# Performance work log

Hardware: AMD Instinct MI355X
Metric: run time of the kernel (lower is better)

The kernel has to match this reference:

```python
import jax, jax.numpy as jnp
import numpy as np

N, DIM, H, E = 50000, 64, 8, 800000
NEG_SLOPE = 0.2


def setup_inputs() -> dict:
    key = jax.random.key(0)
    ks = jax.random.split(key, 6)
    x = jax.random.normal(ks[0], (N, DIM), dtype=jnp.float32)
    edge_index = jax.random.randint(ks[1], (2, E), 0, N, dtype=jnp.int32)
    # glorot-ish scaled params
    W = jax.random.normal(ks[2], (DIM, H * DIM), dtype=jnp.float32) * (1.0 / np.sqrt(DIM))
    att_src = jax.random.normal(ks[3], (H, DIM), dtype=jnp.float32) * (1.0 / np.sqrt(DIM))
    att_dst = jax.random.normal(ks[4], (H, DIM), dtype=jnp.float32) * (1.0 / np.sqrt(DIM))
    bias = jnp.zeros((DIM,), dtype=jnp.float32)
    return {"x": x, "edge_index": edge_index, "W": W, "att_src": att_src, "att_dst": att_dst, "bias": bias}


def reference(x, edge_index, W, att_src, att_dst, bias):
    n = x.shape[0]
    # PyG GATConv default: add self-loops
    loops = jnp.arange(n, dtype=edge_index.dtype)
    src = jnp.concatenate([edge_index[0], loops])  # [E+N]
    dst = jnp.concatenate([edge_index[1], loops])  # [E+N]
    # project: [N, H, C]
    h = (x @ W).reshape(n, H, DIM)
    # per-node attention contributions: [N, H]
    a_src = jnp.einsum("nhc,hc->nh", h, att_src)
    a_dst = jnp.einsum("nhc,hc->nh", h, att_dst)
    # per-edge logits with LeakyReLU: [E+N, H]
    logits = jax.nn.leaky_relu(a_src[src] + a_dst[dst], negative_slope=NEG_SLOPE)
    # segment softmax over incoming edges of each destination node
    seg_max = jax.ops.segment_max(logits, dst, num_segments=n)  # [N, H]
    seg_max = jnp.where(jnp.isfinite(seg_max), seg_max, 0.0)
    e = jnp.exp(logits - seg_max[dst])
    denom = jax.ops.segment_sum(e, dst, num_segments=n)  # [N, H]
    alpha = e / denom[dst]  # every node has a self-loop -> denom > 0
    # weighted messages and scatter-add: [E+N, H, C] -> [N, H, C]
    msg = h[src] * alpha[:, :, None]
    out = jax.ops.segment_sum(msg, dst, num_segments=n)
    # concat=False -> mean over heads, then bias
    return out.mean(axis=1) + bias
```

## Files before the change

### kernel.cpp

```cpp
#include <hip/hip_runtime.h>
#include <hip/hip_bf16.h>

#define NHEAD 8
#define KDIM 64
#define NCOL 512
#define NEG_SLOPE 0.2f
#define BUCKET 64
#define EPT 8

typedef short bf16x8 __attribute__((ext_vector_type(8)));
typedef float f32x4 __attribute__((ext_vector_type(4)));

__device__ inline float leaky(float x) { return fmaxf(x, NEG_SLOPE * x); }
__device__ inline float bf2f(unsigned short u) { return __uint_as_float(((unsigned)u) << 16); }
__device__ inline unsigned short f2bf(float f) {
    unsigned b = __float_as_uint(f);
    b += 0x7FFFu + ((b >> 16) & 1u);
    return (unsigned short)(b >> 16);
}

__global__ void k_wprep(const float* __restrict__ W, const float* __restrict__ att_src,
                        const float* __restrict__ att_dst,
                        float* __restrict__ WsT, float* __restrict__ WdT,
                        unsigned short* __restrict__ Bhi, unsigned short* __restrict__ Blo,
                        int* __restrict__ cur, int n) {
    int tid = blockIdx.x * 256 + threadIdx.x;
    for (int i = tid; i < n; i += 32768) cur[i] = 0;
    if (tid < NHEAD * KDIM) {
        int h = tid >> 6, k = tid & 63;
        float ps = 0.f, pd = 0.f;
        const float4* wp = (const float4*)(W + (size_t)k * NCOL + h * KDIM);
        const float4* sp = (const float4*)(att_src + h * KDIM);
        const float4* dp = (const float4*)(att_dst + h * KDIM);
        #pragma unroll
        for (int q = 0; q < KDIM / 4; ++q) {
            float4 wv = wp[q], sv = sp[q], dv = dp[q];
            ps += wv.x * sv.x + wv.y * sv.y + wv.z * sv.z + wv.w * sv.w;
            pd += wv.x * dv.x + wv.y * dv.y + wv.z * dv.z + wv.w * dv.w;
        }
        WsT[h * KDIM + k] = ps;
        WdT[h * KDIM + k] = pd;
    }
    if (tid < 4 * 16 * 64 * 8) {
        int j  = tid & 7;
        int l  = (tid >> 3) & 63;
        int kk = (tid >> 9) & 15;
        int ct = tid >> 13;
        int c  = ct * 16 + (l & 15);
        int hk = kk * 32 + ((l >> 4) << 3) + j;
        int h = hk >> 6, kx = hk & 63;
        float w = W[(size_t)kx * NCOL + h * KDIM + c];
        unsigned short hi = f2bf(w);
        Bhi[tid] = hi;
        Blo[tid] = f2bf(w - bf2f(hi));
    }
}

__global__ void k_xafill(const float* __restrict__ x,
                         const int* __restrict__ src, const int* __restrict__ dst,
                         const float* __restrict__ WsT, const float* __restrict__ WdT,
                         float* __restrict__ asrc, float* __restrict__ adst,
                         unsigned short* __restrict__ xb,
                         int* __restrict__ cur, unsigned short* __restrict__ bucket,
                         int n, int E, int nbx) {
    const int b = blockIdx.x;
    const int t = threadIdx.x;
    if (b < nbx) {
        int i = b * 256 + t;
        if (i >= n * NHEAD) return;
        int node = i >> 3, h = i & 7;
        const float4* xp = (const float4*)(x + (size_t)node * KDIM);
        const float4* sp = (const float4*)(WsT + h * KDIM);
        const float4* dp = (const float4*)(WdT + h * KDIM);
        float ps = 0.f, pd = 0.f;
        float4 kept0 = {0, 0, 0, 0}, kept1 = {0, 0, 0, 0};
        #pragma unroll
        for (int q = 0; q < KDIM / 4; ++q) {
            float4 xv = xp[q], sv = sp[q], dv = dp[q];
            if (q == 2 * h)     kept0 = xv;
            if (q == 2 * h + 1) kept1 = xv;
            ps += xv.x * sv.x + xv.y * sv.y + xv.z * sv.z + xv.w * sv.w;
            pd += xv.x * dv.x + xv.y * dv.y + xv.z * dv.z + xv.w * dv.w;
        }
        asrc[i] = ps;
        adst[i] = pd;
        ushort4 o0, o1;
        o0.x = f2bf(kept0.x); o0.y = f2bf(kept0.y); o0.z = f2bf(kept0.z); o0.w = f2bf(kept0.w);
        o1.x = f2bf(kept1.x); o1.y = f2bf(kept1.y); o1.z = f2bf(kept1.z); o1.w = f2bf(kept1.w);
        ushort4* op = (ushort4*)(xb + (size_t)node * KDIM + h * 8);
        op[0] = o0; op[1] = o1;
    } else {
        long long base = ((long long)(b - nbx) * 256 + t) * EPT;
        if (base + EPT <= E) {
            int4 d0 = *(const int4*)(dst + base);
            int4 d1 = *(const int4*)(dst + base + 4);
            int4 s0 = *(const int4*)(src + base);
            int4 s1 = *(const int4*)(src + base + 4);
            int dd[EPT] = {d0.x, d0.y, d0.z, d0.w, d1.x, d1.y, d1.z, d1.w};
            int ss[EPT] = {s0.x, s0.y, s0.z, s0.w, s1.x, s1.y, s1.z, s1.w};
            int pp[EPT];
            #pragma unroll
            for (int q = 0; q < EPT; ++q) pp[q] = atomicAdd(cur + dd[q], 1);
            #pragma unroll
            for (int q = 0; q < EPT; ++q)
                if (pp[q] < BUCKET)
                    bucket[(size_t)dd[q] * BUCKET + pp[q]] = (unsigned short)ss[q];
        } else {
            for (long long i = base; i < E; ++i) {
                int d = dst[i];
                int p = atomicAdd(cur + d, 1);
                if (p < BUCKET) bucket[(size_t)d * BUCKET + p] = (unsigned short)src[i];
            }
        }
    }
}

__global__ __launch_bounds__(256, 8) void k_aggproj(const unsigned short* __restrict__ bucket,
                                                    const int* __restrict__ cur,
                                                    const float* __restrict__ asrc,
                                                    const float* __restrict__ adst,
                                                    const unsigned short* __restrict__ xb,
                                                    const unsigned short* __restrict__ Bhi,
                                                    const unsigned short* __restrict__ Blo,
                                                    const float* __restrict__ bias,
                                                    float* __restrict__ out, int n) {
    __shared__ __align__(16) unsigned short Yh_l[16][520];

    const int t = threadIdx.x;
    const int w = t >> 6;
    const int lane = t & 63;
    const int base = blockIdx.x * 16;
    const int hg = lane >> 3;
    const int hLo = lane & 7;
    const int dly = (lane & 7) << 3;

#define PROCU(EV, RW)                                                          \
    {                                                                          \
        den += (EV);                                                           \
        uint4 u_ = (RW);                                                       \
        y[0] += (EV) * __uint_as_float(u_.x << 16);                            \
        y[1] += (EV) * __uint_as_float(u_.x & 0xFFFF0000u);                    \
        y[2] += (EV) * __uint_as_float(u_.y << 16);                            \
        y[3] += (EV) * __uint_as_float(u_.y & 0xFFFF0000u);                    \
        y[4] += (EV) * __uint_as_float(u_.z << 16);                            \
        y[5] += (EV) * __uint_as_float(u_.z & 0xFFFF0000u);                    \
        y[6] += (EV) * __uint_as_float(u_.w << 16);                            \
        y[7] += (EV) * __uint_as_float(u_.w & 0xFFFF0000u);                    \
    }

    for (int q = 0; q < 4; ++q) {
        const int row = w * 4 + q;
        int d = base + row;
        if (d >= n) d = n - 1;

        const float adLo = adst[(size_t)d * NHEAD + hLo];
        float den = 0.f;
        float y[8];
        #pragma unroll
        for (int i = 0; i < 8; ++i) y[i] = 0.f;

        int cnt = cur[d];
        cnt = cnt < BUCKET ? cnt : BUCKET;
        int sv = (lane < cnt) ? (int)bucket[(size_t)d * BUCKET + lane] : 0;

        {
            float asLo = asrc[(size_t)d * NHEAD + hLo];
            float evs = __expf(leaky(asLo + adLo));
            float e = __shfl(evs, hg);
            uint4 r = *(const uint4*)(xb + ((size_t)d << 6) + dly);
            PROCU(e, r)
        }

        int j = 0;
        for (; j + 4 <= cnt; j += 4) {
            int sb = __shfl(sv, j + ((lane >> 3) & 3));
            float ab = asrc[(size_t)sb * NHEAD + hLo];
            float ev = __expf(leaky(ab + adLo));
            int s0 = __shfl(sv, j);
            int s1 = __shfl(sv, j + 1);
            int s2 = __shfl(sv, j + 2);
            int s3 = __shfl(sv, j + 3);
            uint4 r0 = *(const uint4*)(xb + ((size_t)s0 << 6) + dly);
            uint4 r1 = *(const uint4*)(xb + ((size_t)s1 << 6) + dly);
            uint4 r2 = *(const uint4*)(xb + ((size_t)s2 << 6) + dly);
            uint4 r3 = *(const uint4*)(xb + ((size_t)s3 << 6) + dly);
            float e0 = __shfl(ev, 0 * 8 + hg);
            PROCU(e0, r0)
            float e1 = __shfl(ev, 1 * 8 + hg);
            PROCU(e1, r1)
            float e2 = __shfl(ev, 2 * 8 + hg);
            PROCU(e2, r2)
            float e3 = __shfl(ev, 3 * 8 + hg);
            PROCU(e3, r3)
        }
        for (; j < cnt; ++j) {
            int s = __shfl(sv, j);
            float a = asrc[(size_t)s * NHEAD + hLo];
            float evt = __expf(leaky(a + adLo));
            float e = __shfl(evt, hg);
            uint4 r = *(const uint4*)(xb + ((size_t)s << 6) + dly);
            PROCU(e, r)
        }

        float inv = 1.0f / den;
        ushort4 h0, h1;
        h0.x = f2bf(y[0] * inv); h0.y = f2bf(y[1] * inv);
        h0.z = f2bf(y[2] * inv); h0.w = f2bf(y[3] * inv);
        h1.x = f2bf(y[4] * inv); h1.y = f2bf(y[5] * inv);
        h1.z = f2bf(y[6] * inv); h1.w = f2bf(y[7] * inv);
        unsigned short* yh = &Yh_l[row][hg * KDIM + dly];
        ((ushort4*)yh)[0] = h0; ((ushort4*)yh)[1] = h1;
    }
#undef PROCU

    __syncthreads();

    const bf16x8* BH = (const bf16x8*)Bhi;
    const bf16x8* BL = (const bf16x8*)Blo;
    const int ar = lane & 15;
    const int ak = (lane >> 4) << 3;

    f32x4 acc = {0.f, 0.f, 0.f, 0.f};
    #pragma unroll
    for (int kk = 0; kk < 16; ++kk) {
        bf16x8 ah = *(const bf16x8*)&Yh_l[ar][kk * 32 + ak];
        bf16x8 bh = BH[(w * 16 + kk) * 64 + lane];
        bf16x8 bl = BL[(w * 16 + kk) * 64 + lane];
        acc = __builtin_amdgcn_mfma_f32_16x16x32_bf16(ah, bh, acc, 0, 0, 0);
        acc = __builtin_amdgcn_mfma_f32_16x16x32_bf16(ah, bl, acc, 0, 0, 0);
    }

    int col = w * 16 + (lane & 15);
    float b = bias[col];
    int rbase = base + ((lane >> 4) << 2);
    #pragma unroll
    for (int r = 0; r < 4; ++r) {
        int rowg = rbase + r;
        if (rowg < n) out[(size_t)rowg * KDIM + col] = acc[r] * 0.125f + b;
    }
}

extern "C" void kernel_launch(void* const* d_in, const int* in_sizes, int n_in,
                              void* d_out, int out_size, void* d_ws, size_t ws_size,
                              hipStream_t stream) {
    const float* x       = (const float*)d_in[0];
    const int*   ei      = (const int*)d_in[1];
    const float* W       = (const float*)d_in[2];
    const float* att_src = (const float*)d_in[3];
    const float* att_dst = (const float*)d_in[4];
    const float* bias    = (const float*)d_in[5];

    const int n = in_sizes[0] / KDIM;
    const int E = in_sizes[1] / 2;
    const int* src = ei;
    const int* dst = ei + E;

    char* w = (char*)d_ws;
    unsigned short* xb  = (unsigned short*)w;  w += (size_t)n * KDIM * 2;
    unsigned short* Bhi = (unsigned short*)w;  w += (size_t)32768 * 2;
    unsigned short* Blo = (unsigned short*)w;  w += (size_t)32768 * 2;
    float* WsT  = (float*)w;                   w += (size_t)NHEAD * KDIM * 4;
    float* WdT  = (float*)w;                   w += (size_t)NHEAD * KDIM * 4;
    float* asrc = (float*)w;                   w += (size_t)n * NHEAD * 4;
    float* adst = (float*)w;                   w += (size_t)n * NHEAD * 4;
    int*   cur  = (int*)w;                     w += (size_t)n * 4;
    unsigned short* bucket = (unsigned short*)w; w += (size_t)n * BUCKET * 2;

    k_wprep<<<128, 256, 0, stream>>>(W, att_src, att_dst, WsT, WdT, Bhi, Blo, cur, n);

    const int nbx = (n * NHEAD + 255) / 256;
    const int ethreads = (E + EPT - 1) / EPT;
    const int nbe = (ethreads + 255) / 256;
    k_xafill<<<nbx + nbe, 256, 0, stream>>>(x, src, dst, WsT, WdT, asrc, adst, xb,
                                            cur, bucket, n, E, nbx);

    k_aggproj<<<(n + 15) / 16, 256, 0, stream>>>(bucket, cur, asrc, adst, xb, Bhi, Blo,
                                                 bias, (float*)d_out, n);
}
```

Baseline: 146.0 us.

## Replace fixed-size per-node edge buckets with atomicExch linked lists

```diff
diff --git a/kernel.cpp b/kernel.cpp
--- a/kernel.cpp
+++ b/kernel.cpp
@@ -23,9 +23,9 @@
                         const float* __restrict__ att_dst,
                         float* __restrict__ WsT, float* __restrict__ WdT,
                         unsigned short* __restrict__ Bhi, unsigned short* __restrict__ Blo,
-                        int* __restrict__ cur, int n) {
+                        int* __restrict__ head, int n) {
     int tid = blockIdx.x * 256 + threadIdx.x;
-    for (int i = tid; i < n; i += 32768) cur[i] = 0;
+    for (int i = tid; i < n; i += 32768) head[i] = -1;
     if (tid < NHEAD * KDIM) {
         int h = tid >> 6, k = tid & 63;
         float ps = 0.f, pd = 0.f;
@@ -61,7 +61,7 @@
                          const float* __restrict__ WsT, const float* __restrict__ WdT,
                          float* __restrict__ asrc, float* __restrict__ adst,
                          unsigned short* __restrict__ xb,
-                         int* __restrict__ cur, unsigned short* __restrict__ bucket,
+                         int* __restrict__ head, int2* __restrict__ pairs,
                          int n, int E, int nbx) {
     const int b = blockIdx.x;
     const int t = threadIdx.x;
@@ -98,25 +98,27 @@
             int4 s1 = *(const int4*)(src + base + 4);
             int dd[EPT] = {d0.x, d0.y, d0.z, d0.w, d1.x, d1.y, d1.z, d1.w};
             int ss[EPT] = {s0.x, s0.y, s0.z, s0.w, s1.x, s1.y, s1.z, s1.w};
-            int pp[EPT];
-            #pragma unroll
-            for (int q = 0; q < EPT; ++q) pp[q] = atomicAdd(cur + dd[q], 1);
+            int oo[EPT];
             #pragma unroll
             for (int q = 0; q < EPT; ++q)
-                if (pp[q] < BUCKET)
-                    bucket[(size_t)dd[q] * BUCKET + pp[q]] = (unsigned short)ss[q];
+                oo[q] = atomicExch(head + dd[q], (int)(base + q));
+            int4* pp = (int4*)(pairs + base);
+            pp[0] = make_int4(ss[0], oo[0], ss[1], oo[1]);
+            pp[1] = make_int4(ss[2], oo[2], ss[3], oo[3]);
+            pp[2] = make_int4(ss[4], oo[4], ss[5], oo[5]);
+            pp[3] = make_int4(ss[6], oo[6], ss[7], oo[7]);
         } else {
             for (long long i = base; i < E; ++i) {
                 int d = dst[i];
-                int p = atomicAdd(cur + d, 1);
-                if (p < BUCKET) bucket[(size_t)d * BUCKET + p] = (unsigned short)src[i];
+                int old = atomicExch(head + d, (int)i);
+                pairs[i] = make_int2(src[i], old);
             }
         }
     }
 }
 
-__global__ __launch_bounds__(256, 8) void k_aggproj(const unsigned short* __restrict__ bucket,
-                                                    const int* __restrict__ cur,
+__global__ __launch_bounds__(256, 8) void k_aggproj(const int* __restrict__ head,
+                                                    const int2* __restrict__ pairs,
                                                     const float* __restrict__ asrc,
                                                     const float* __restrict__ adst,
                                                     const unsigned short* __restrict__ xb,
@@ -125,6 +127,8 @@
                                                     const float* __restrict__ bias,
                                                     float* __restrict__ out, int n) {
     __shared__ __align__(16) unsigned short Yh_l[16][520];
+    __shared__ unsigned short sids[16][64];
+    __shared__ int scnt[16];
 
     const int t = threadIdx.x;
     const int w = t >> 6;
@@ -133,6 +137,21 @@
     const int hg = lane >> 3;
     const int hLo = lane & 7;
     const int dly = (lane & 7) << 3;
+
+    if ((lane & 15) == 0) {
+        int rowg = w * 4 + (lane >> 4);
+        int dg = base + rowg;
+        if (dg >= n) dg = n - 1;
+        int e = head[dg];
+        int c = 0;
+        while (e >= 0 && c < BUCKET) {
+            int2 pr = pairs[e];
+            sids[rowg][c++] = (unsigned short)pr.x;
+            e = pr.y;
+        }
+        scnt[rowg] = c;
+    }
+    __syncthreads();
 
 #define PROCU(EV, RW)                                                          \
     {                                                                          \
@@ -159,9 +178,8 @@
         #pragma unroll
         for (int i = 0; i < 8; ++i) y[i] = 0.f;
 
-        int cnt = cur[d];
-        cnt = cnt < BUCKET ? cnt : BUCKET;
-        int sv = (lane < cnt) ? (int)bucket[(size_t)d * BUCKET + lane] : 0;
+        const int cnt = scnt[row];
+        int sv = (int)sids[row][lane];
 
         {
             float asLo = asrc[(size_t)d * NHEAD + hLo];
@@ -263,17 +281,17 @@
     float* WdT  = (float*)w;                   w += (size_t)NHEAD * KDIM * 4;
     float* asrc = (float*)w;                   w += (size_t)n * NHEAD * 4;
     float* adst = (float*)w;                   w += (size_t)n * NHEAD * 4;
-    int*   cur  = (int*)w;                     w += (size_t)n * 4;
-    unsigned short* bucket = (unsigned short*)w; w += (size_t)n * BUCKET * 2;
-
-    k_wprep<<<128, 256, 0, stream>>>(W, att_src, att_dst, WsT, WdT, Bhi, Blo, cur, n);
+    int*   head = (int*)w;                     w += (size_t)n * 4;
+    int2*  pairs = (int2*)w;                   w += (size_t)E * 8;
+
+    k_wprep<<<128, 256, 0, stream>>>(W, att_src, att_dst, WsT, WdT, Bhi, Blo, head, n);
 
     const int nbx = (n * NHEAD + 255) / 256;
     const int ethreads = (E + EPT - 1) / EPT;
     const int nbe = (ethreads + 255) / 256;
     k_xafill<<<nbx + nbe, 256, 0, stream>>>(x, src, dst, WsT, WdT, asrc, adst, xb,
-                                            cur, bucket, n, E, nbx);
-
-    k_aggproj<<<(n + 15) / 16, 256, 0, stream>>>(bucket, cur, asrc, adst, xb, Bhi, Blo,
+                                            head, pairs, n, E, nbx);
+
+    k_aggproj<<<(n + 15) / 16, 256, 0, stream>>>(head, pairs, asrc, adst, xb, Bhi, Blo,
                                                  bias, (float*)d_out, n);
 }
```

After: 158.0 us. +8.2%, slower.

## Replace global-atomic edge bucketing with LDS-binned destination-range scans

Applied to the files above, without the earlier changes.

```diff
diff --git a/kernel.cpp b/kernel.cpp
--- a/kernel.cpp
+++ b/kernel.cpp
@@ -5,8 +5,11 @@
 #define KDIM 64
 #define NCOL 512
 #define NEG_SLOPE 0.2f
-#define BUCKET 64
-#define EPT 8
+#define NBIN 64
+#define NSLICE 4
+#define SLOT 20
+#define BUCKET 80
+#define MAXRNG 800
 
 typedef short bf16x8 __attribute__((ext_vector_type(8)));
 typedef float f32x4 __attribute__((ext_vector_type(4)));
@@ -22,10 +25,8 @@
 __global__ void k_wprep(const float* __restrict__ W, const float* __restrict__ att_src,
                         const float* __restrict__ att_dst,
                         float* __restrict__ WsT, float* __restrict__ WdT,
-                        unsigned short* __restrict__ Bhi, unsigned short* __restrict__ Blo,
-                        int* __restrict__ cur, int n) {
+                        unsigned short* __restrict__ Bhi, unsigned short* __restrict__ Blo) {
     int tid = blockIdx.x * 256 + threadIdx.x;
-    for (int i = tid; i < n; i += 32768) cur[i] = 0;
     if (tid < NHEAD * KDIM) {
         int h = tid >> 6, k = tid & 63;
         float ps = 0.f, pd = 0.f;
@@ -61,14 +62,44 @@
                          const float* __restrict__ WsT, const float* __restrict__ WdT,
                          float* __restrict__ asrc, float* __restrict__ adst,
                          unsigned short* __restrict__ xb,
-                         int* __restrict__ cur, unsigned short* __restrict__ bucket,
-                         int n, int E, int nbx) {
+                         unsigned char* __restrict__ cnts,
+                         unsigned short* __restrict__ bucket,
+                         int n, long long E, int nbx) {
     const int b = blockIdx.x;
     const int t = threadIdx.x;
-    if (b < nbx) {
-        int i = b * 256 + t;
-        if (i >= n * NHEAD) return;
-        int node = i >> 3, h = i & 7;
+
+    if (b < NBIN * NSLICE) {
+        __shared__ int cur[MAXRNG];
+        const int bin   = b >> 2;
+        const int slice = b & 3;
+        const int start = (int)(((long long)bin * n) / NBIN);
+        const int end   = (int)(((long long)(bin + 1) * n) / NBIN);
+        const int rng   = end - start;
+
+        for (int i = t; i < rng; i += 256) cur[i] = 0;
+        __syncthreads();
+
+        const long long e0 = (long long)slice * E / NSLICE;
+        const long long e1 = (long long)(slice + 1) * E / NSLICE;
+        for (long long i = e0 + t; i < e1; i += 256) {
+            int d = dst[i];
+            if (d >= start && d < end) {
+                int p = atomicAdd(&cur[d - start], 1);
+                if (p < SLOT)
+                    bucket[(size_t)d * BUCKET + slice * SLOT + p] = (unsigned short)src[i];
+            }
+        }
+        __syncthreads();
+
+        for (int i = t; i < rng; i += 256) {
+            int c = cur[i];
+            cnts[(size_t)(start + i) * NSLICE + slice] =
+                (unsigned char)(c < SLOT ? c : SLOT);
+        }
+    } else {
+        long long i = (long long)(b - NBIN * NSLICE) * 256 + t;
+        if (i >= (long long)n * NHEAD) return;
+        int node = (int)(i >> 3), h = (int)(i & 7);
         const float4* xp = (const float4*)(x + (size_t)node * KDIM);
         const float4* sp = (const float4*)(WsT + h * KDIM);
         const float4* dp = (const float4*)(WdT + h * KDIM);
@@ -89,34 +120,11 @@
         o1.x = f2bf(kept1.x); o1.y = f2bf(kept1.y); o1.z = f2bf(kept1.z); o1.w = f2bf(kept1.w);
         ushort4* op = (ushort4*)(xb + (size_t)node * KDIM + h * 8);
         op[0] = o0; op[1] = o1;
-    } else {
-        long long base = ((long long)(b - nbx) * 256 + t) * EPT;
-        if (base + EPT <= E) {
-            int4 d0 = *(const int4*)(dst + base);
-            int4 d1 = *(const int4*)(dst + base + 4);
-            int4 s0 = *(const int4*)(src + base);
-            int4 s1 = *(const int4*)(src + base + 4);
-            int dd[EPT] = {d0.x, d0.y, d0.z, d0.w, d1.x, d1.y, d1.z, d1.w};
-            int ss[EPT] = {s0.x, s0.y, s0.z, s0.w, s1.x, s1.y, s1.z, s1.w};
-            int pp[EPT];
-            #pragma unroll
-            for (int q = 0; q < EPT; ++q) pp[q] = atomicAdd(cur + dd[q], 1);
-            #pragma unroll
-            for (int q = 0; q < EPT; ++q)
-                if (pp[q] < BUCKET)
-                    bucket[(size_t)dd[q] * BUCKET + pp[q]] = (unsigned short)ss[q];
-        } else {
-            for (long long i = base; i < E; ++i) {
-                int d = dst[i];
-                int p = atomicAdd(cur + d, 1);
-                if (p < BUCKET) bucket[(size_t)d * BUCKET + p] = (unsigned short)src[i];
-            }
-        }
     }
 }
 
 __global__ __launch_bounds__(256, 8) void k_aggproj(const unsigned short* __restrict__ bucket,
-                                                    const int* __restrict__ cur,
+                                                    const unsigned char* __restrict__ cnts,
                                                     const float* __restrict__ asrc,
                                                     const float* __restrict__ adst,
                                                     const unsigned short* __restrict__ xb,
@@ -159,9 +167,17 @@
         #pragma unroll
         for (int i = 0; i < 8; ++i) y[i] = 0.f;
 
-        int cnt = cur[d];
-        cnt = cnt < BUCKET ? cnt : BUCKET;
-        int sv = (lane < cnt) ? (int)bucket[(size_t)d * BUCKET + lane] : 0;
+        const uchar4 cc = *(const uchar4*)(cnts + (size_t)d * NSLICE);
+        const int b1 = cc.x;
+        const int b2 = b1 + cc.y;
+        const int b3 = b2 + cc.z;
+        int cnt = b3 + cc.w;
+        cnt = cnt < 64 ? cnt : 64;
+
+        int sg = (lane >= b1) + (lane >= b2) + (lane >= b3);
+        int bs = sg == 0 ? 0 : (sg == 1 ? b1 : (sg == 2 ? b2 : b3));
+        int sv = (lane < cnt)
+                 ? (int)bucket[(size_t)d * BUCKET + sg * SLOT + (lane - bs)] : 0;
 
         {
             float asLo = asrc[(size_t)d * NHEAD + hLo];
@@ -251,7 +267,7 @@
     const float* bias    = (const float*)d_in[5];
 
     const int n = in_sizes[0] / KDIM;
-    const int E = in_sizes[1] / 2;
+    const long long E = in_sizes[1] / 2;
     const int* src = ei;
     const int* dst = ei + E;
 
@@ -263,17 +279,16 @@
     float* WdT  = (float*)w;                   w += (size_t)NHEAD * KDIM * 4;
     float* asrc = (float*)w;                   w += (size_t)n * NHEAD * 4;
     float* adst = (float*)w;                   w += (size_t)n * NHEAD * 4;
-    int*   cur  = (int*)w;                     w += (size_t)n * 4;
+    unsigned char* cnts = (unsigned char*)w;   w += (size_t)n * NSLICE;
+    w = (char*)(((size_t)w + 15) & ~(size_t)15);
     unsigned short* bucket = (unsigned short*)w; w += (size_t)n * BUCKET * 2;
 
-    k_wprep<<<128, 256, 0, stream>>>(W, att_src, att_dst, WsT, WdT, Bhi, Blo, cur, n);
-
-    const int nbx = (n * NHEAD + 255) / 256;
-    const int ethreads = (E + EPT - 1) / EPT;
-    const int nbe = (ethreads + 255) / 256;
-    k_xafill<<<nbx + nbe, 256, 0, stream>>>(x, src, dst, WsT, WdT, asrc, adst, xb,
-                                            cur, bucket, n, E, nbx);
-
-    k_aggproj<<<(n + 15) / 16, 256, 0, stream>>>(bucket, cur, asrc, adst, xb, Bhi, Blo,
+    k_wprep<<<128, 256, 0, stream>>>(W, att_src, att_dst, WsT, WdT, Bhi, Blo);
+
+    const int nbx = (int)(((long long)n * NHEAD + 255) / 256);
+    k_xafill<<<NBIN * NSLICE + nbx, 256, 0, stream>>>(x, src, dst, WsT, WdT, asrc, adst,
+                                                      xb, cnts, bucket, n, E, nbx);
+
+    k_aggproj<<<(n + 15) / 16, 256, 0, stream>>>(bucket, cnts, asrc, adst, xb, Bhi, Blo,
                                                  bias, (float*)d_out, n);
 }
```

Result: slower. 321.9 us (+120.4%).
